# Optimization experiments

Hardware: AMD Instinct MI355X
Metric: run time of the kernel (lower is better)

## Reference

```python
import jax, jax.numpy as jnp
import numpy as np

N, E, HID, NS, NC, NCLS, NG = 100000, 1200000, 64, 16, 8, 2, 512
EPS = 1e-5


def setup_inputs() -> dict:
    key = jax.random.key(0)
    ks = jax.random.split(key, 16)
    inp = {
        "shape_id": jax.random.randint(ks[0], (N,), 0, NS),
        "colour_id": jax.random.randint(ks[1], (N,), 0, NC),
        "edge_index": jax.random.randint(ks[2], (2, E), 0, N),
        "batch": jnp.sort(jax.random.randint(ks[3], (N,), 0, NG)),
        # embeddings
        "shape_W": jax.random.normal(ks[4], (NS, HID), jnp.float32) * 0.02,
        "col_W": jax.random.normal(ks[5], (NC, HID), jnp.float32) * 0.02,
        # SAGEConv 1: lin_l (on aggregated neighbors, with bias), lin_r (on self, no bias)
        "W1l": jax.random.normal(ks[6], (HID, HID), jnp.float32) * 0.05,
        "b1": jnp.zeros((HID,), jnp.float32),
        "W1r": jax.random.normal(ks[7], (HID, HID), jnp.float32) * 0.05,
        "g1": jnp.ones((HID,), jnp.float32),
        "be1": jnp.zeros((HID,), jnp.float32),
        # SAGEConv 2
        "W2l": jax.random.normal(ks[8], (HID, HID), jnp.float32) * 0.05,
        "b2": jnp.zeros((HID,), jnp.float32),
        "W2r": jax.random.normal(ks[9], (HID, HID), jnp.float32) * 0.05,
        "g2": jnp.ones((HID,), jnp.float32),
        "be2": jnp.zeros((HID,), jnp.float32),
        # classifier
        "Wlin": jax.random.normal(ks[10], (HID, NCLS), jnp.float32) * 0.05,
        "blin": jnp.zeros((NCLS,), jnp.float32),
    }
    return inp


def _sage(x, edge_index, Wl, bl, Wr):
    # PyG SAGEConv with mean aggregation: lin_l(mean_{j in N(i)} x_j) + lin_r(x_i)
    src, dst = edge_index[0], edge_index[1]
    n = x.shape[0]
    msg_sum = jax.ops.segment_sum(x[src], dst, num_segments=n)  # [N, HID]
    cnt = jax.ops.segment_sum(jnp.ones((src.shape[0],), x.dtype), dst, num_segments=n)
    mean = msg_sum / jnp.maximum(cnt, 1.0)[:, None]
    return mean @ Wl + bl + x @ Wr


def _bn(x, gamma, beta):
    # batch-statistics normalization over node dim (training-mode BatchNorm1d)
    mu = x.mean(0)
    var = x.var(0)
    return (x - mu) * jax.lax.rsqrt(var + EPS) * gamma + beta


def reference(shape_id, colour_id, edge_index, batch,
              shape_W, col_W, W1l, b1, W1r, g1, be1,
              W2l, b2, W2r, g2, be2, Wlin, blin):
    x = shape_W[shape_id] + col_W[colour_id]                  # [N, HID]
    x = jax.nn.relu(_bn(_sage(x, edge_index, W1l, b1, W1r), g1, be1))
    # dropout(0.3) treated as identity (eval mode)
    x = jax.nn.relu(_bn(_sage(x, edge_index, W2l, b2, W2r), g2, be2))
    graph_x = jax.ops.segment_sum(x, batch, num_segments=NG)  # global_add_pool
    return graph_x @ Wlin + blin                              # [NG, NCLS]
```

## Files before the change

kernel.cpp:

```cpp
#include <hip/hip_runtime.h>
#include <stdint.h>

#define N_NODES 100000
#define N_EDGES 1200000
#define HID 64
#define NGRAPH 512
#define NCLS 2
#define BN_EPS 1e-5f

#define NTILES (N_NODES / 16)
#define NBLK_G2 782

#define BKT_SH 8
#define BKT_NODES 256
#define NB 391
#define BKT_CAP 4080
#define EB_PER_BLK 4096
#define NBLK_E 293

typedef __attribute__((ext_vector_type(8))) short short8;
typedef __attribute__((ext_vector_type(4))) float f32x4;

__device__ inline float bf2f(uint32_t hi16) {
    uint32_t u = hi16 << 16;
    return __builtin_bit_cast(float, u);
}
__device__ inline uint32_t f2bf_rtn(float f) {
    uint32_t u = __builtin_bit_cast(uint32_t, f);
    return (u + 0x7FFFu + ((u >> 16) & 1u)) >> 16;
}

__global__ void k_code(const int* __restrict__ sid, const int* __restrict__ cid,
                       unsigned char* __restrict__ code8) {
    int i = blockIdx.x * blockDim.x + threadIdx.x;
    if (i < N_NODES) code8[i] = (unsigned char)(sid[i] | (cid[i] << 4));
}

__global__ __launch_bounds__(256) void k_tab(const float* __restrict__ sW,
                                             const float* __restrict__ cW,
                                             const float* __restrict__ W1l,
                                             const float* __restrict__ W1r,
                                             const float* __restrict__ b1,
                                             float* __restrict__ TsL,
                                             ushort* __restrict__ tblR) {
    int gid = blockIdx.x * 256 + threadIdx.x;
    if (gid < 24 * 64) {
        int row = gid >> 6, d = gid & 63;
        const float* e = (row < 16) ? &sW[row * 64] : &cW[(row - 16) * 64];
        float acc = 0.f;
        #pragma unroll 8
        for (int k = 0; k < 64; ++k) acc += e[k] * W1l[k * 64 + d];
        TsL[gid] = acc;
    } else if (gid < 24 * 64 + 128 * 64) {
        int r = gid - 24 * 64;
        int c = r >> 6, d = r & 63;
        int s = c & 15, cl = c >> 4;
        float acc = b1[d];
        #pragma unroll 8
        for (int k = 0; k < 64; ++k)
            acc += (sW[s * 64 + k] + cW[cl * 64 + k]) * W1r[k * 64 + d];
        tblR[r] = (ushort)f2bf_rtn(acc);
    }
}

__global__ __launch_bounds__(256) void k_bucket(const int* __restrict__ src,
                                                const int* __restrict__ dst,
                                                const unsigned char* __restrict__ code8,
                                                int* __restrict__ bucket_cnt,
                                                uint32_t* __restrict__ staged) {
    __shared__ int h[NB];
    __shared__ int cur[NB];
    int tid = threadIdx.x;
    for (int j = tid; j < NB; j += 256) h[j] = 0;
    __syncthreads();
    uint32_t pk[16];
    int bk[16];
    int base = blockIdx.x * EB_PER_BLK;
    #pragma unroll
    for (int i = 0; i < 16; ++i) {
        int e = base + i * 256 + tid;
        if (e < N_EDGES) {
            int s = src[e], d = dst[e];
            int c = code8[s];
            bk[i] = d >> BKT_SH;
            pk[i] = ((uint32_t)c << 25) | ((uint32_t)s << 8)
                  | (uint32_t)(d & (BKT_NODES - 1));
            atomicAdd(&h[bk[i]], 1);
        } else {
            bk[i] = -1;
        }
    }
    __syncthreads();
    for (int j = tid; j < NB; j += 256)
        cur[j] = (h[j] > 0) ? atomicAdd(&bucket_cnt[j], h[j]) : 0;
    __syncthreads();
    #pragma unroll
    for (int i = 0; i < 16; ++i) {
        if (bk[i] >= 0) {
            int slot = atomicAdd(&cur[bk[i]], 1);
            staged[(size_t)bk[i] * BKT_CAP + slot] = pk[i];
        }
    }
}

__global__ __launch_bounds__(512) void k_bscan(const int* __restrict__ bucket_cnt,
                                               int* __restrict__ bucket_off,
                                               int* __restrict__ row_ptr) {
    __shared__ int sh[512];
    int t = threadIdx.x;
    int v = (t < NB) ? bucket_cnt[t] : 0;
    sh[t] = v;
    __syncthreads();
    #pragma unroll
    for (int off = 1; off < 512; off <<= 1) {
        int cur = sh[t];
        int u = (t >= off) ? sh[t - off] : 0;
        __syncthreads();
        sh[t] = cur + u;
        __syncthreads();
    }
    if (t < NB) bucket_off[t] = sh[t] - v;
    if (t == 0) {
        bucket_off[NB] = N_EDGES;
        row_ptr[N_NODES] = N_EDGES;
    }
}

__global__ __launch_bounds__(256) void k_place(const uint32_t* __restrict__ staged,
                                               const int* __restrict__ bucket_off,
                                               const unsigned char* __restrict__ code8,
                                               const float* __restrict__ TsL,
                                               const ushort* __restrict__ tblR,
                                               int* __restrict__ row_ptr,
                                               int* __restrict__ csr_src,
                                               ushort* __restrict__ h1b,
                                               float* __restrict__ sums,
                                               float* __restrict__ sumsq) {
    __shared__ int hist[BKT_NODES];
    __shared__ int cursor[BKT_NODES];
    __shared__ int part[256];
    __shared__ int cnt24[BKT_NODES * 12];
    __shared__ float lsum[4][64];
    __shared__ float lsq[4][64];
    int b = blockIdx.x;
    int tid = threadIdx.x;
    int lane = tid & 63, wv = tid >> 6;
    int cc = tid & 15;
    int nodes0 = b << BKT_SH;
    int nn = min(BKT_NODES, N_NODES - nodes0);
    int ebeg = bucket_off[b];
    int cntb = bucket_off[b + 1] - ebeg;
    const uint32_t* st = &staged[(size_t)b * BKT_CAP];

    f32x4 trow[24];
    #pragma unroll
    for (int s = 0; s < 24; ++s)
        trow[s] = *(const f32x4*)&TsL[s * 64 + cc * 4];

    hist[tid] = 0;
    #pragma unroll
    for (int j = 0; j < 12; ++j) cnt24[tid * 12 + j] = 0;
    __syncthreads();
    for (int e = tid; e < cntb; e += 256)
        atomicAdd(&hist[(int)(st[e] & (BKT_NODES - 1))], 1);
    __syncthreads();
    int myc = hist[tid];
    part[tid] = myc;
    __syncthreads();
    #pragma unroll
    for (int off = 1; off < 256; off <<= 1) {
        int curv = part[tid];
        int u = (tid >= off) ? part[tid - off] : 0;
        __syncthreads();
        part[tid] = curv + u;
        __syncthreads();
    }
    int ex = ebeg + part[tid] - myc;
    cursor[tid] = ex;
    if (tid < nn) row_ptr[nodes0 + tid] = ex;
    __syncthreads();
    for (int e = tid; e < cntb; e += 256) {
        uint32_t pk = st[e];
        int nl = (int)(pk & (BKT_NODES - 1));
        int slot = atomicAdd(&cursor[nl], 1);
        csr_src[slot] = (int)((pk >> 8) & 0x1FFFFu);
        int c = (int)(pk >> 25);
        int sb = c & 15, cb = c >> 4;
        atomicAdd(&cnt24[nl * 12 + (sb >> 1)], 1 << ((sb & 1) * 16));
        atomicAdd(&cnt24[nl * 12 + 8 + (cb >> 1)], 1 << ((cb & 1) * 16));
    }
    __syncthreads();

    float sv0 = 0, sv1 = 0, sv2 = 0, sv3 = 0;
    float qv0 = 0, qv1 = 0, qv2 = 0, qv3 = 0;
    int nrow = tid >> 4;
    for (int it = 0; it < 16; ++it) {
        int nl = it * 16 + nrow;
        if (nl >= nn) continue;
        int node = nodes0 + nl;
        int cw[12];
        *(uint4*)&cw[0] = *(const uint4*)&cnt24[nl * 12];
        *(uint4*)&cw[4] = *(const uint4*)&cnt24[nl * 12 + 4];
        *(uint4*)&cw[8] = *(const uint4*)&cnt24[nl * 12 + 8];
        int deg = hist[nl];
        float a0 = 0, a1 = 0, a2 = 0, a3 = 0;
        #pragma unroll
        for (int ss = 0; ss < 24; ++ss) {
            int j = (ss < 16) ? (ss >> 1) : (8 + ((ss - 16) >> 1));
            float w = (float)((cw[j] >> ((ss & 1) * 16)) & 0xFFFF);
            a0 += w * trow[ss].x; a1 += w * trow[ss].y;
            a2 += w * trow[ss].z; a3 += w * trow[ss].w;
        }
        float inv = 1.f / (float)max(deg, 1);
        int ci = code8[node];
        uint2 trv = *(const uint2*)&tblR[ci * 64 + cc * 4];
        float h0 = fmaf(a0, inv, bf2f(trv.x & 0xFFFFu));
        float h1 = fmaf(a1, inv, bf2f(trv.x >> 16));
        float h2 = fmaf(a2, inv, bf2f(trv.y & 0xFFFFu));
        float h3 = fmaf(a3, inv, bf2f(trv.y >> 16));
        uint2 o;
        o.x = f2bf_rtn(h0) | (f2bf_rtn(h1) << 16);
        o.y = f2bf_rtn(h2) | (f2bf_rtn(h3) << 16);
        *(uint2*)&h1b[(size_t)node * HID + cc * 4] = o;
        sv0 += h0; qv0 += h0 * h0;
        sv1 += h1; qv1 += h1 * h1;
        sv2 += h2; qv2 += h2 * h2;
        sv3 += h3; qv3 += h3 * h3;
    }
    sv0 += __shfl_xor(sv0, 16); sv0 += __shfl_xor(sv0, 32);
    sv1 += __shfl_xor(sv1, 16); sv1 += __shfl_xor(sv1, 32);
    sv2 += __shfl_xor(sv2, 16); sv2 += __shfl_xor(sv2, 32);
    sv3 += __shfl_xor(sv3, 16); sv3 += __shfl_xor(sv3, 32);
    qv0 += __shfl_xor(qv0, 16); qv0 += __shfl_xor(qv0, 32);
    qv1 += __shfl_xor(qv1, 16); qv1 += __shfl_xor(qv1, 32);
    qv2 += __shfl_xor(qv2, 16); qv2 += __shfl_xor(qv2, 32);
    qv3 += __shfl_xor(qv3, 16); qv3 += __shfl_xor(qv3, 32);
    if ((lane >> 4) == 0) {
        lsum[wv][cc * 4 + 0] = sv0; lsum[wv][cc * 4 + 1] = sv1;
        lsum[wv][cc * 4 + 2] = sv2; lsum[wv][cc * 4 + 3] = sv3;
        lsq[wv][cc * 4 + 0] = qv0; lsq[wv][cc * 4 + 1] = qv1;
        lsq[wv][cc * 4 + 2] = qv2; lsq[wv][cc * 4 + 3] = qv3;
    }
    __syncthreads();
    if (wv == 0) {
        int d = lane;
        float S = lsum[0][d] + lsum[1][d] + lsum[2][d] + lsum[3][d];
        float Q = lsq[0][d] + lsq[1][d] + lsq[2][d] + lsq[3][d];
        atomicAdd(&sums[d], S);
        atomicAdd(&sumsq[d], Q);
    }
}

__global__ void k_bn_params(const float* __restrict__ sums, const float* __restrict__ sumsq,
                            const float* __restrict__ g, const float* __restrict__ be,
                            float* __restrict__ scale, float* __restrict__ shift) {
    int d = threadIdx.x;
    if (d >= HID) return;
    float mu  = sums[d] * (1.f / N_NODES);
    float var = sumsq[d] * (1.f / N_NODES) - mu * mu;
    float sc  = g[d] * rsqrtf(var + BN_EPS);
    scale[d] = sc;
    shift[d] = be[d] - mu * sc;
}

__global__ __launch_bounds__(256) void k_gather2(
    const ushort* __restrict__ h1b, const int* __restrict__ row_ptr,
    const int* __restrict__ csr_src,
    const float* __restrict__ scale, const float* __restrict__ shift,
    ushort* __restrict__ meanb) {
    int c = blockIdx.x;
    int x = c & 7, m = c >> 3;
    int blk = x + 8 * (m >> 3);
    if (blk >= NBLK_G2) return;
    int chunk16 = 8 * blk + (m & 7);
    if (chunk16 >= NTILES) return;
    int lane = threadIdx.x & 63, wv = threadIdx.x >> 6;
    int g = lane >> 3, cc = lane & 7;
    float4 sc0 = *(const float4*)&scale[cc * 8];
    float4 sc1 = *(const float4*)&scale[cc * 8 + 4];
    float4 sh0 = *(const float4*)&shift[cc * 8];
    float4 sh1 = *(const float4*)&shift[cc * 8 + 4];
    const uint4* x4 = (const uint4*)h1b;
    uint4* mb4 = (uint4*)meanb;
    for (int n = 0; n < 4; ++n) {
        int node = chunk16 * 16 + wv * 4 + n;
        int beg = row_ptr[node], end = row_ptr[node + 1];
        int deg = end - beg;
        float a0 = 0, a1 = 0, a2 = 0, a3 = 0, a4 = 0, a5 = 0, a6 = 0, a7 = 0;
        float b0 = 0, b1 = 0, b2 = 0, b3 = 0, b4 = 0, b5 = 0, b6 = 0, b7 = 0;
        int iters = (deg + 15) >> 4;
        for (int it = 0; it < iters; ++it) {
            int ea = beg + it * 16 + g;
            int eb = ea + 8;
            if (ea < end) {
                int sn = csr_src[ea];
                uint4 u = x4[(size_t)sn * 8 + cc];
                a0 += fmaxf(fmaf(bf2f(u.x & 0xFFFFu), sc0.x, sh0.x), 0.f);
                a1 += fmaxf(fmaf(bf2f(u.x >> 16),     sc0.y, sh0.y), 0.f);
                a2 += fmaxf(fmaf(bf2f(u.y & 0xFFFFu), sc0.z, sh0.z), 0.f);
                a3 += fmaxf(fmaf(bf2f(u.y >> 16),     sc0.w, sh0.w), 0.f);
                a4 += fmaxf(fmaf(bf2f(u.z & 0xFFFFu), sc1.x, sh1.x), 0.f);
                a5 += fmaxf(fmaf(bf2f(u.z >> 16),     sc1.y, sh1.y), 0.f);
                a6 += fmaxf(fmaf(bf2f(u.w & 0xFFFFu), sc1.z, sh1.z), 0.f);
                a7 += fmaxf(fmaf(bf2f(u.w >> 16),     sc1.w, sh1.w), 0.f);
            }
            if (eb < end) {
                int sn = csr_src[eb];
                uint4 u = x4[(size_t)sn * 8 + cc];
                b0 += fmaxf(fmaf(bf2f(u.x & 0xFFFFu), sc0.x, sh0.x), 0.f);
                b1 += fmaxf(fmaf(bf2f(u.x >> 16),     sc0.y, sh0.y), 0.f);
                b2 += fmaxf(fmaf(bf2f(u.y & 0xFFFFu), sc0.z, sh0.z), 0.f);
                b3 += fmaxf(fmaf(bf2f(u.y >> 16),     sc0.w, sh0.w), 0.f);
                b4 += fmaxf(fmaf(bf2f(u.z & 0xFFFFu), sc1.x, sh1.x), 0.f);
                b5 += fmaxf(fmaf(bf2f(u.z >> 16),     sc1.y, sh1.y), 0.f);
                b6 += fmaxf(fmaf(bf2f(u.w & 0xFFFFu), sc1.z, sh1.z), 0.f);
                b7 += fmaxf(fmaf(bf2f(u.w >> 16),     sc1.w, sh1.w), 0.f);
            }
        }
        a0 += b0; a1 += b1; a2 += b2; a3 += b3;
        a4 += b4; a5 += b5; a6 += b6; a7 += b7;
        #pragma unroll
        for (int off = 8; off < 64; off <<= 1) {
            a0 += __shfl_xor(a0, off); a1 += __shfl_xor(a1, off);
            a2 += __shfl_xor(a2, off); a3 += __shfl_xor(a3, off);
            a4 += __shfl_xor(a4, off); a5 += __shfl_xor(a5, off);
            a6 += __shfl_xor(a6, off); a7 += __shfl_xor(a7, off);
        }
        if (lane < 8) {
            float inv = 1.f / (float)max(deg, 1);
            uint4 o;
            o.x = f2bf_rtn(a0 * inv) | (f2bf_rtn(a1 * inv) << 16);
            o.y = f2bf_rtn(a2 * inv) | (f2bf_rtn(a3 * inv) << 16);
            o.z = f2bf_rtn(a4 * inv) | (f2bf_rtn(a5 * inv) << 16);
            o.w = f2bf_rtn(a6 * inv) | (f2bf_rtn(a7 * inv) << 16);
            mb4[(size_t)node * 8 + lane] = o;
        }
    }
}

__global__ void k_wpack(const float* __restrict__ Wl, const float* __restrict__ Wr,
                        ushort* __restrict__ wpk) {
    int gid = blockIdx.x * blockDim.x + threadIdx.x;
    if (gid >= 1024) return;
    int tile = gid >> 6;
    int lane = gid & 63;
    int nt = tile >> 2, kt = tile & 3;
    #pragma unroll
    for (int j = 0; j < 8; ++j) {
        int k = kt * 32 + (lane >> 4) * 8 + j;
        int n = nt * 16 + (lane & 15);
        float v = (k < 64) ? Wl[k * HID + n] : Wr[(k - 64) * HID + n];
        wpk[(size_t)(tile * 64 + lane) * 8 + j] = (ushort)f2bf_rtn(v);
    }
}

__global__ __launch_bounds__(256) void k_gemm2(
    const ushort* __restrict__ meanb, const ushort* __restrict__ h1b,
    const ushort* __restrict__ wpk, const float* __restrict__ bias,
    const float* __restrict__ scale, const float* __restrict__ shift,
    ushort* __restrict__ hout, float* __restrict__ sums, float* __restrict__ sumsq) {
    __shared__ float lsum[4][64];
    __shared__ float lsq[4][64];
    int lane = threadIdx.x & 63;
    int wv = threadIdx.x >> 6;
    int r16 = lane & 15;
    int grp = lane >> 4;
    short8 bfrag[4][4];
    const short8* wp = (const short8*)wpk;
    #pragma unroll
    for (int nt = 0; nt < 4; ++nt)
        #pragma unroll
        for (int kt = 0; kt < 4; ++kt)
            bfrag[nt][kt] = wp[(nt * 4 + kt) * 64 + lane];
    float bcol[4];
    #pragma unroll
    for (int nt = 0; nt < 4; ++nt) bcol[nt] = bias[nt * 16 + r16];
    float4 scA0 = *(const float4*)&scale[grp * 8];
    float4 scA1 = *(const float4*)&scale[grp * 8 + 4];
    float4 shA0 = *(const float4*)&shift[grp * 8];
    float4 shA1 = *(const float4*)&shift[grp * 8 + 4];
    float4 scB0 = *(const float4*)&scale[32 + grp * 8];
    float4 scB1 = *(const float4*)&scale[32 + grp * 8 + 4];
    float4 shB0 = *(const float4*)&shift[32 + grp * 8];
    float4 shB1 = *(const float4*)&shift[32 + grp * 8 + 4];

    int tbase = (blockIdx.x * 4 + wv) * 2;
    int t0 = tbase, t1 = tbase + 1;
    bool v0 = t0 < NTILES, v1 = t1 < NTILES;

    short8 am0[2], am1[2];
    uint2 u0[4], u1[4];
    if (v0) {
        int node = t0 * 16 + r16;
        const short8* mrow = (const short8*)(meanb + (size_t)node * HID);
        am0[0] = mrow[grp];
        am0[1] = mrow[4 + grp];
        const uint2* s2 = (const uint2*)(h1b + (size_t)node * HID);
        u0[0] = s2[grp * 2]; u0[1] = s2[grp * 2 + 1];
        u0[2] = s2[8 + grp * 2]; u0[3] = s2[9 + grp * 2];
    }
    if (v1) {
        int node = t1 * 16 + r16;
        const short8* mrow = (const short8*)(meanb + (size_t)node * HID);
        am1[0] = mrow[grp];
        am1[1] = mrow[4 + grp];
        const uint2* s2 = (const uint2*)(h1b + (size_t)node * HID);
        u1[0] = s2[grp * 2]; u1[1] = s2[grp * 2 + 1];
        u1[2] = s2[8 + grp * 2]; u1[3] = s2[9 + grp * 2];
    }

    float sv[4] = {0.f, 0.f, 0.f, 0.f}, qv[4] = {0.f, 0.f, 0.f, 0.f};

    #pragma unroll
    for (int j = 0; j < 2; ++j) {
        bool valid = j == 0 ? v0 : v1;
        if (!valid) continue;
        int tile = j == 0 ? t0 : t1;
        short8* amp = j == 0 ? am0 : am1;
        uint2* up = j == 0 ? u0 : u1;
        short8 a2v, a3v;
        a2v[0] = (short)f2bf_rtn(fmaxf(fmaf(bf2f(up[0].x & 0xFFFFu), scA0.x, shA0.x), 0.f));
        a2v[1] = (short)f2bf_rtn(fmaxf(fmaf(bf2f(up[0].x >> 16),     scA0.y, shA0.y), 0.f));
        a2v[2] = (short)f2bf_rtn(fmaxf(fmaf(bf2f(up[0].y & 0xFFFFu), scA0.z, shA0.z), 0.f));
        a2v[3] = (short)f2bf_rtn(fmaxf(fmaf(bf2f(up[0].y >> 16),     scA0.w, shA0.w), 0.f));
        a2v[4] = (short)f2bf_rtn(fmaxf(fmaf(bf2f(up[1].x & 0xFFFFu), scA1.x, shA1.x), 0.f));
        a2v[5] = (short)f2bf_rtn(fmaxf(fmaf(bf2f(up[1].x >> 16),     scA1.y, shA1.y), 0.f));
        a2v[6] = (short)f2bf_rtn(fmaxf(fmaf(bf2f(up[1].y & 0xFFFFu), scA1.z, shA1.z), 0.f));
        a2v[7] = (short)f2bf_rtn(fmaxf(fmaf(bf2f(up[1].y >> 16),     scA1.w, shA1.w), 0.f));
        a3v[0] = (short)f2bf_rtn(fmaxf(fmaf(bf2f(up[2].x & 0xFFFFu), scB0.x, shB0.x), 0.f));
        a3v[1] = (short)f2bf_rtn(fmaxf(fmaf(bf2f(up[2].x >> 16),     scB0.y, shB0.y), 0.f));
        a3v[2] = (short)f2bf_rtn(fmaxf(fmaf(bf2f(up[2].y & 0xFFFFu), scB0.z, shB0.z), 0.f));
        a3v[3] = (short)f2bf_rtn(fmaxf(fmaf(bf2f(up[2].y >> 16),     scB0.w, shB0.w), 0.f));
        a3v[4] = (short)f2bf_rtn(fmaxf(fmaf(bf2f(up[3].x & 0xFFFFu), scB1.x, shB1.x), 0.f));
        a3v[5] = (short)f2bf_rtn(fmaxf(fmaf(bf2f(up[3].x >> 16),     scB1.y, shB1.y), 0.f));
        a3v[6] = (short)f2bf_rtn(fmaxf(fmaf(bf2f(up[3].y & 0xFFFFu), scB1.z, shB1.z), 0.f));
        a3v[7] = (short)f2bf_rtn(fmaxf(fmaf(bf2f(up[3].y >> 16),     scB1.w, shB1.w), 0.f));
        short8 a[4];
        a[0] = amp[0];
        a[1] = amp[1];
        a[2] = a2v;
        a[3] = a3v;
        f32x4 acc[4];
        #pragma unroll
        for (int nt = 0; nt < 4; ++nt) acc[nt] = (f32x4){0.f, 0.f, 0.f, 0.f};
        #pragma unroll
        for (int nt = 0; nt < 4; ++nt)
            #pragma unroll
            for (int kt = 0; kt < 4; ++kt)
                acc[nt] = __builtin_amdgcn_mfma_f32_16x16x32_bf16(a[kt], bfrag[nt][kt],
                                                                  acc[nt], 0, 0, 0);
        #pragma unroll
        for (int nt = 0; nt < 4; ++nt) {
            #pragma unroll
            for (int r = 0; r < 4; ++r) {
                float hv = acc[nt][r] + bcol[nt];
                int rrow = tile * 16 + grp * 4 + r;
                hout[(size_t)rrow * HID + nt * 16 + r16] = (ushort)f2bf_rtn(hv);
                sv[nt] += hv;
                qv[nt] += hv * hv;
            }
        }
    }
    #pragma unroll
    for (int nt = 0; nt < 4; ++nt) {
        float v = sv[nt];
        v += __shfl_xor(v, 16); v += __shfl_xor(v, 32);
        float q = qv[nt];
        q += __shfl_xor(q, 16); q += __shfl_xor(q, 32);
        if (grp == 0) {
            lsum[wv][nt * 16 + r16] = v;
            lsq[wv][nt * 16 + r16] = q;
        }
    }
    __syncthreads();
    if (wv == 0) {
        int d = lane;
        float S = lsum[0][d] + lsum[1][d] + lsum[2][d] + lsum[3][d];
        float Q = lsq[0][d] + lsq[1][d] + lsq[2][d] + lsq[3][d];
        atomicAdd(&sums[d], S);
        atomicAdd(&sumsq[d], Q);
    }
}

__global__ __launch_bounds__(256) void k_pool(const ushort* __restrict__ h,
                                              const int* __restrict__ batch,
                                              const float* __restrict__ scale,
                                              const float* __restrict__ shift,
                                              float* __restrict__ graph_x) {
    int wv = threadIdx.x >> 6, d = threadIdx.x & 63;
    float sc = scale[d], sh = shift[d];
    const int NCHUNK = 4096;
    int cidx = blockIdx.x * 4 + wv;
    int chunk = (N_NODES + NCHUNK - 1) / NCHUNK;
    int a = cidx * chunk;
    int b = min(a + chunk, N_NODES);
    if (a >= b) return;
    int cur = batch[a];
    float acc = 0.f;
    for (int i = a; i < b; ++i) {
        int g = batch[i];
        if (g != cur) {
            atomicAdd(&graph_x[cur * HID + d], acc);
            acc = 0.f;
            cur = g;
        }
        float v = bf2f((uint32_t)h[(size_t)i * HID + d]);
        acc += fmaxf(fmaf(v, sc, sh), 0.f);
    }
    atomicAdd(&graph_x[cur * HID + d], acc);
}

__global__ void k_cls(const float* __restrict__ graph_x, const float* __restrict__ Wlin,
                      const float* __restrict__ blin, float* __restrict__ out) {
    int idx = blockIdx.x * blockDim.x + threadIdx.x;
    if (idx >= NGRAPH * NCLS) return;
    int g = idx / NCLS, c = idx % NCLS;
    float acc = blin[c];
    #pragma unroll
    for (int k = 0; k < HID; ++k) acc += graph_x[g * HID + k] * Wlin[k * NCLS + c];
    out[idx] = acc;
}

extern "C" void kernel_launch(void* const* d_in, const int* in_sizes, int n_in,
                              void* d_out, int out_size, void* d_ws, size_t ws_size,
                              hipStream_t stream) {
    const int*   sid   = (const int*)d_in[0];
    const int*   cid   = (const int*)d_in[1];
    const int*   esrc  = (const int*)d_in[2];
    const int*   edst  = esrc + N_EDGES;
    const int*   batch = (const int*)d_in[3];
    const float* sW    = (const float*)d_in[4];
    const float* cW    = (const float*)d_in[5];
    const float* W1l   = (const float*)d_in[6];
    const float* b1    = (const float*)d_in[7];
    const float* W1r   = (const float*)d_in[8];
    const float* g1    = (const float*)d_in[9];
    const float* be1   = (const float*)d_in[10];
    const float* W2l   = (const float*)d_in[11];
    const float* b2    = (const float*)d_in[12];
    const float* W2r   = (const float*)d_in[13];
    const float* g2    = (const float*)d_in[14];
    const float* be2   = (const float*)d_in[15];
    const float* Wlin  = (const float*)d_in[16];
    const float* blin  = (const float*)d_in[17];
    float* out = (float*)d_out;

    const size_t FEAT = (size_t)N_NODES * HID;
    ushort* scratch = (ushort*)d_ws;
    ushort* h1b   = scratch + FEAT;
    ushort* h2b   = h1b + FEAT;
    ushort* wpk2  = h2b + FEAT;
    ushort* tblR  = wpk2 + 8192;
    float* TsL    = (float*)(tblR + 8192);
    float* fp     = TsL + 24 * 64;
    float* sums1  = fp;            float* sumsq1 = sums1 + HID;
    float* sums2  = sumsq1 + HID;  float* sumsq2 = sums2 + HID;
    float* scale1 = sumsq2 + HID;  float* shift1 = scale1 + HID;
    float* scale2 = shift1 + HID;  float* shift2 = scale2 + HID;
    float* graph_x = shift2 + HID;
    int* row_ptr  = (int*)(graph_x + (size_t)NGRAPH * HID);
    int* csr_src  = row_ptr + N_NODES + 1;
    int* bucket_cnt = csr_src + N_EDGES;
    int* bucket_off = bucket_cnt + NB;
    unsigned char* code8 = (unsigned char*)(bucket_off + NB + 1);
    uint32_t* staged = (uint32_t*)scratch;
    ushort* meanb = scratch;

    hipMemsetAsync(bucket_cnt, 0, NB * sizeof(int), stream);
    hipMemsetAsync(sums1, 0, 4 * HID * sizeof(float), stream);
    hipMemsetAsync(graph_x, 0, (size_t)NGRAPH * HID * sizeof(float), stream);

    k_code<<<(N_NODES + 255) / 256, 256, 0, stream>>>(sid, cid, code8);
    k_tab<<<38, 256, 0, stream>>>(sW, cW, W1l, W1r, b1, TsL, tblR);
    k_wpack<<<4, 256, 0, stream>>>(W2l, W2r, wpk2);

    k_bucket<<<NBLK_E, 256, 0, stream>>>(esrc, edst, code8, bucket_cnt, staged);
    k_bscan<<<1, 512, 0, stream>>>(bucket_cnt, bucket_off, row_ptr);
    k_place<<<NB, 256, 0, stream>>>(staged, bucket_off, code8, TsL, tblR,
                                    row_ptr, csr_src, h1b, sums1, sumsq1);
    k_bn_params<<<1, 64, 0, stream>>>(sums1, sumsq1, g1, be1, scale1, shift1);

    k_gather2<<<8 * 784, 256, 0, stream>>>(h1b, row_ptr, csr_src, scale1, shift1, meanb);
    k_gemm2<<<NBLK_G2, 256, 0, stream>>>(meanb, h1b, wpk2, b2, scale1, shift1,
                                         h2b, sums2, sumsq2);
    k_bn_params<<<1, 64, 0, stream>>>(sums2, sumsq2, g2, be2, scale2, shift2);

    k_pool<<<1024, 256, 0, stream>>>(h2b, batch, scale2, shift2, graph_x);
    k_cls<<<(NGRAPH * NCLS + 255) / 256, 256, 0, stream>>>(graph_x, Wlin, blin, out);
}
```

Before: 167.2 us.

## Precompute BN1+ReLU activations once per node and fold memsets into kernels

Adds a k_act kernel that applies layer-1 batch-norm and ReLU once per node and stores bf16 activations, so the neighbor gather and gemm2 read ready activations instead of recomputing BN+ReLU on every edge. The memsets of bucket counts, BN stats and graph_x are moved into k_code and k_act to avoid separate memset launches. The trade-off is an extra full-feature read and write pass plus a new kernel launch, and the gather now averages activations that were already rounded to bf16.

```diff
diff --git a/kernel.cpp b/kernel.cpp
--- a/kernel.cpp
+++ b/kernel.cpp
@@ -31,9 +31,14 @@
 }
 
 __global__ void k_code(const int* __restrict__ sid, const int* __restrict__ cid,
-                       unsigned char* __restrict__ code8) {
+                       unsigned char* __restrict__ code8,
+                       int* __restrict__ bucket_cnt, float* __restrict__ stats) {
     int i = blockIdx.x * blockDim.x + threadIdx.x;
     if (i < N_NODES) code8[i] = (unsigned char)(sid[i] | (cid[i] << 4));
+    if (blockIdx.x == 0) {
+        for (int j = threadIdx.x; j < NB; j += 256) bucket_cnt[j] = 0;
+        for (int j = threadIdx.x; j < 4 * HID; j += 256) stats[j] = 0.f;
+    }
 }
 
 __global__ __launch_bounds__(256) void k_tab(const float* __restrict__ sW,
@@ -263,11 +268,31 @@
     shift[d] = be[d] - mu * sc;
 }
 
+__global__ void k_act(const ushort* __restrict__ h, const float* __restrict__ scale,
+                      const float* __restrict__ shift, ushort* __restrict__ act,
+                      float* __restrict__ graph_x) {
+    if (blockIdx.x == 0) {
+        for (int j = threadIdx.x; j < NGRAPH * HID; j += 256) graph_x[j] = 0.f;
+    }
+    int t = blockIdx.x * blockDim.x + threadIdx.x;
+    if (t >= N_NODES * 16) return;
+    int q = t & 15;
+    uint2 u = *(const uint2*)&h[(size_t)t * 4];
+    float4 sc = *(const float4*)&scale[q * 4];
+    float4 sh = *(const float4*)&shift[q * 4];
+    float f0 = fmaxf(fmaf(bf2f(u.x & 0xFFFFu), sc.x, sh.x), 0.f);
+    float f1 = fmaxf(fmaf(bf2f(u.x >> 16),     sc.y, sh.y), 0.f);
+    float f2 = fmaxf(fmaf(bf2f(u.y & 0xFFFFu), sc.z, sh.z), 0.f);
+    float f3 = fmaxf(fmaf(bf2f(u.y >> 16),     sc.w, sh.w), 0.f);
+    uint2 o;
+    o.x = f2bf_rtn(f0) | (f2bf_rtn(f1) << 16);
+    o.y = f2bf_rtn(f2) | (f2bf_rtn(f3) << 16);
+    *(uint2*)&act[(size_t)t * 4] = o;
+}
+
 __global__ __launch_bounds__(256) void k_gather2(
-    const ushort* __restrict__ h1b, const int* __restrict__ row_ptr,
-    const int* __restrict__ csr_src,
-    const float* __restrict__ scale, const float* __restrict__ shift,
-    ushort* __restrict__ meanb) {
+    const ushort* __restrict__ act1b, const int* __restrict__ row_ptr,
+    const int* __restrict__ csr_src, ushort* __restrict__ meanb) {
     int c = blockIdx.x;
     int x = c & 7, m = c >> 3;
     int blk = x + 8 * (m >> 3);
@@ -276,11 +301,7 @@
     if (chunk16 >= NTILES) return;
     int lane = threadIdx.x & 63, wv = threadIdx.x >> 6;
     int g = lane >> 3, cc = lane & 7;
-    float4 sc0 = *(const float4*)&scale[cc * 8];
-    float4 sc1 = *(const float4*)&scale[cc * 8 + 4];
-    float4 sh0 = *(const float4*)&shift[cc * 8];
-    float4 sh1 = *(const float4*)&shift[cc * 8 + 4];
-    const uint4* x4 = (const uint4*)h1b;
+    const uint4* x4 = (const uint4*)act1b;
     uint4* mb4 = (uint4*)meanb;
     for (int n = 0; n < 4; ++n) {
         int node = chunk16 * 16 + wv * 4 + n;
@@ -295,26 +316,26 @@
             if (ea < end) {
                 int sn = csr_src[ea];
                 uint4 u = x4[(size_t)sn * 8 + cc];
-                a0 += fmaxf(fmaf(bf2f(u.x & 0xFFFFu), sc0.x, sh0.x), 0.f);
-                a1 += fmaxf(fmaf(bf2f(u.x >> 16),     sc0.y, sh0.y), 0.f);
-                a2 += fmaxf(fmaf(bf2f(u.y & 0xFFFFu), sc0.z, sh0.z), 0.f);
-                a3 += fmaxf(fmaf(bf2f(u.y >> 16),     sc0.w, sh0.w), 0.f);
-                a4 += fmaxf(fmaf(bf2f(u.z & 0xFFFFu), sc1.x, sh1.x), 0.f);
-                a5 += fmaxf(fmaf(bf2f(u.z >> 16),     sc1.y, sh1.y), 0.f);
-                a6 += fmaxf(fmaf(bf2f(u.w & 0xFFFFu), sc1.z, sh1.z), 0.f);
-                a7 += fmaxf(fmaf(bf2f(u.w >> 16),     sc1.w, sh1.w), 0.f);
+                a0 += bf2f(u.x & 0xFFFFu);
+                a1 += bf2f(u.x >> 16);
+                a2 += bf2f(u.y & 0xFFFFu);
+                a3 += bf2f(u.y >> 16);
+                a4 += bf2f(u.z & 0xFFFFu);
+                a5 += bf2f(u.z >> 16);
+                a6 += bf2f(u.w & 0xFFFFu);
+                a7 += bf2f(u.w >> 16);
             }
             if (eb < end) {
                 int sn = csr_src[eb];
                 uint4 u = x4[(size_t)sn * 8 + cc];
-                b0 += fmaxf(fmaf(bf2f(u.x & 0xFFFFu), sc0.x, sh0.x), 0.f);
-                b1 += fmaxf(fmaf(bf2f(u.x >> 16),     sc0.y, sh0.y), 0.f);
-                b2 += fmaxf(fmaf(bf2f(u.y & 0xFFFFu), sc0.z, sh0.z), 0.f);
-                b3 += fmaxf(fmaf(bf2f(u.y >> 16),     sc0.w, sh0.w), 0.f);
-                b4 += fmaxf(fmaf(bf2f(u.z & 0xFFFFu), sc1.x, sh1.x), 0.f);
-                b5 += fmaxf(fmaf(bf2f(u.z >> 16),     sc1.y, sh1.y), 0.f);
-                b6 += fmaxf(fmaf(bf2f(u.w & 0xFFFFu), sc1.z, sh1.z), 0.f);
-                b7 += fmaxf(fmaf(bf2f(u.w >> 16),     sc1.w, sh1.w), 0.f);
+                b0 += bf2f(u.x & 0xFFFFu);
+                b1 += bf2f(u.x >> 16);
+                b2 += bf2f(u.y & 0xFFFFu);
+                b3 += bf2f(u.y >> 16);
+                b4 += bf2f(u.z & 0xFFFFu);
+                b5 += bf2f(u.z >> 16);
+                b6 += bf2f(u.w & 0xFFFFu);
+                b7 += bf2f(u.w >> 16);
             }
         }
         a0 += b0; a1 += b1; a2 += b2; a3 += b3;
@@ -355,9 +376,8 @@
 }
 
 __global__ __launch_bounds__(256) void k_gemm2(
-    const ushort* __restrict__ meanb, const ushort* __restrict__ h1b,
+    const ushort* __restrict__ meanb, const ushort* __restrict__ act1b,
     const ushort* __restrict__ wpk, const float* __restrict__ bias,
-    const float* __restrict__ scale, const float* __restrict__ shift,
     ushort* __restrict__ hout, float* __restrict__ sums, float* __restrict__ sumsq) {
     __shared__ float lsum[4][64];
     __shared__ float lsq[4][64];
@@ -375,38 +395,29 @@
     float bcol[4];
     #pragma unroll
     for (int nt = 0; nt < 4; ++nt) bcol[nt] = bias[nt * 16 + r16];
-    float4 scA0 = *(const float4*)&scale[grp * 8];
-    float4 scA1 = *(const float4*)&scale[grp * 8 + 4];
-    float4 shA0 = *(const float4*)&shift[grp * 8];
-    float4 shA1 = *(const float4*)&shift[grp * 8 + 4];
-    float4 scB0 = *(const float4*)&scale[32 + grp * 8];
-    float4 scB1 = *(const float4*)&scale[32 + grp * 8 + 4];
-    float4 shB0 = *(const float4*)&shift[32 + grp * 8];
-    float4 shB1 = *(const float4*)&shift[32 + grp * 8 + 4];
 
     int tbase = (blockIdx.x * 4 + wv) * 2;
     int t0 = tbase, t1 = tbase + 1;
     bool v0 = t0 < NTILES, v1 = t1 < NTILES;
 
-    short8 am0[2], am1[2];
-    uint2 u0[4], u1[4];
+    short8 a0arr[4], a1arr[4];
     if (v0) {
         int node = t0 * 16 + r16;
         const short8* mrow = (const short8*)(meanb + (size_t)node * HID);
-        am0[0] = mrow[grp];
-        am0[1] = mrow[4 + grp];
-        const uint2* s2 = (const uint2*)(h1b + (size_t)node * HID);
-        u0[0] = s2[grp * 2]; u0[1] = s2[grp * 2 + 1];
-        u0[2] = s2[8 + grp * 2]; u0[3] = s2[9 + grp * 2];
+        const short8* srow = (const short8*)(act1b + (size_t)node * HID);
+        a0arr[0] = mrow[grp];
+        a0arr[1] = mrow[4 + grp];
+        a0arr[2] = srow[grp];
+        a0arr[3] = srow[4 + grp];
     }
     if (v1) {
         int node = t1 * 16 + r16;
         const short8* mrow = (const short8*)(meanb + (size_t)node * HID);
-        am1[0] = mrow[grp];
-        am1[1] = mrow[4 + grp];
-        const uint2* s2 = (const uint2*)(h1b + (size_t)node * HID);
-        u1[0] = s2[grp * 2]; u1[1] = s2[grp * 2 + 1];
-        u1[2] = s2[8 + grp * 2]; u1[3] = s2[9 + grp * 2];
+        const short8* srow = (const short8*)(act1b + (size_t)node * HID);
+        a1arr[0] = mrow[grp];
+        a1arr[1] = mrow[4 + grp];
+        a1arr[2] = srow[grp];
+        a1arr[3] = srow[4 + grp];
     }
 
     float sv[4] = {0.f, 0.f, 0.f, 0.f}, qv[4] = {0.f, 0.f, 0.f, 0.f};
@@ -416,30 +427,7 @@
         bool valid = j == 0 ? v0 : v1;
         if (!valid) continue;
         int tile = j == 0 ? t0 : t1;
-        short8* amp = j == 0 ? am0 : am1;
-        uint2* up = j == 0 ? u0 : u1;
-        short8 a2v, a3v;
-        a2v[0] = (short)f2bf_rtn(fmaxf(fmaf(bf2f(up[0].x & 0xFFFFu), scA0.x, shA0.x), 0.f));
-        a2v[1] = (short)f2bf_rtn(fmaxf(fmaf(bf2f(up[0].x >> 16),     scA0.y, shA0.y), 0.f));
-        a2v[2] = (short)f2bf_rtn(fmaxf(fmaf(bf2f(up[0].y & 0xFFFFu), scA0.z, shA0.z), 0.f));
-        a2v[3] = (short)f2bf_rtn(fmaxf(fmaf(bf2f(up[0].y >> 16),     scA0.w, shA0.w), 0.f));
-        a2v[4] = (short)f2bf_rtn(fmaxf(fmaf(bf2f(up[1].x & 0xFFFFu), scA1.x, shA1.x), 0.f));
-        a2v[5] = (short)f2bf_rtn(fmaxf(fmaf(bf2f(up[1].x >> 16),     scA1.y, shA1.y), 0.f));
-        a2v[6] = (short)f2bf_rtn(fmaxf(fmaf(bf2f(up[1].y & 0xFFFFu), scA1.z, shA1.z), 0.f));
-        a2v[7] = (short)f2bf_rtn(fmaxf(fmaf(bf2f(up[1].y >> 16),     scA1.w, shA1.w), 0.f));
-        a3v[0] = (short)f2bf_rtn(fmaxf(fmaf(bf2f(up[2].x & 0xFFFFu), scB0.x, shB0.x), 0.f));
-        a3v[1] = (short)f2bf_rtn(fmaxf(fmaf(bf2f(up[2].x >> 16),     scB0.y, shB0.y), 0.f));
-        a3v[2] = (short)f2bf_rtn(fmaxf(fmaf(bf2f(up[2].y & 0xFFFFu), scB0.z, shB0.z), 0.f));
-        a3v[3] = (short)f2bf_rtn(fmaxf(fmaf(bf2f(up[2].y >> 16),     scB0.w, shB0.w), 0.f));
-        a3v[4] = (short)f2bf_rtn(fmaxf(fmaf(bf2f(up[3].x & 0xFFFFu), scB1.x, shB1.x), 0.f));
-        a3v[5] = (short)f2bf_rtn(fmaxf(fmaf(bf2f(up[3].x >> 16),     scB1.y, shB1.y), 0.f));
-        a3v[6] = (short)f2bf_rtn(fmaxf(fmaf(bf2f(up[3].y & 0xFFFFu), scB1.z, shB1.z), 0.f));
-        a3v[7] = (short)f2bf_rtn(fmaxf(fmaf(bf2f(up[3].y >> 16),     scB1.w, shB1.w), 0.f));
-        short8 a[4];
-        a[0] = amp[0];
-        a[1] = amp[1];
-        a[2] = a2v;
-        a[3] = a3v;
+        short8* a = j == 0 ? a0arr : a1arr;
         f32x4 acc[4];
         #pragma unroll
         for (int nt = 0; nt < 4; ++nt) acc[nt] = (f32x4){0.f, 0.f, 0.f, 0.f};
@@ -548,7 +536,8 @@
     const size_t FEAT = (size_t)N_NODES * HID;
     ushort* scratch = (ushort*)d_ws;
     ushort* h1b   = scratch + FEAT;
-    ushort* h2b   = h1b + FEAT;
+    ushort* act1b = h1b + FEAT;
+    ushort* h2b   = act1b + FEAT;
     ushort* wpk2  = h2b + FEAT;
     ushort* tblR  = wpk2 + 8192;
     float* TsL    = (float*)(tblR + 8192);
@@ -566,11 +555,8 @@
     uint32_t* staged = (uint32_t*)scratch;
     ushort* meanb = scratch;
 
-    hipMemsetAsync(bucket_cnt, 0, NB * sizeof(int), stream);
-    hipMemsetAsync(sums1, 0, 4 * HID * sizeof(float), stream);
-    hipMemsetAsync(graph_x, 0, (size_t)NGRAPH * HID * sizeof(float), stream);
-
-    k_code<<<(N_NODES + 255) / 256, 256, 0, stream>>>(sid, cid, code8);
+    k_code<<<(N_NODES + 255) / 256, 256, 0, stream>>>(sid, cid, code8,
+                                                      bucket_cnt, sums1);
     k_tab<<<38, 256, 0, stream>>>(sW, cW, W1l, W1r, b1, TsL, tblR);
     k_wpack<<<4, 256, 0, stream>>>(W2l, W2r, wpk2);
 
@@ -580,8 +566,11 @@
                                     row_ptr, csr_src, h1b, sums1, sumsq1);
     k_bn_params<<<1, 64, 0, stream>>>(sums1, sumsq1, g1, be1, scale1, shift1);
 
-    k_gather2<<<8 * 784, 256, 0, stream>>>(h1b, row_ptr, csr_src, scale1, shift1, meanb);
-    k_gemm2<<<NBLK_G2, 256, 0, stream>>>(meanb, h1b, wpk2, b2, scale1, shift1,
+    k_act<<<(N_NODES * 16 + 255) / 256, 256, 0, stream>>>(h1b, scale1, shift1,
+                                                          act1b, graph_x);
+
+    k_gather2<<<8 * 784, 256, 0, stream>>>(act1b, row_ptr, csr_src, meanb);
+    k_gemm2<<<NBLK_G2, 256, 0, stream>>>(meanb, act1b, wpk2, b2,
                                          h2b, sums2, sumsq2);
     k_bn_params<<<1, 64, 0, stream>>>(sums2, sumsq2, g2, be2, scale2, shift2);
 
```

After: 162.5 us. -2.8%, faster.
